# Performance work log

Measured on AMD Instinct MI355X. Metric: run time of the kernel, lower is better.

The kernel has to match this reference:

```python
import jax, jax.numpy as jnp
import numpy as np

EPS = 0.001
WEIGHT = 1.0


def _grid_sample_zeros(x, grid):
    """Bilinear grid_sample, align_corners=True, zeros padding.
    x: [B,C,H,W], grid: [B,H,W,2] in [-1,1] (x then y). Returns [B,C,H,W]."""
    B, C, H, W = x.shape
    gx = (grid[..., 0] + 1.0) * 0.5 * (W - 1)  # [B,H,W] pixel coords
    gy = (grid[..., 1] + 1.0) * 0.5 * (H - 1)
    x0 = jnp.floor(gx)
    y0 = jnp.floor(gy)
    x1 = x0 + 1.0
    y1 = y0 + 1.0
    wx1 = gx - x0
    wx0 = 1.0 - wx1
    wy1 = gy - y0
    wy0 = 1.0 - wy1

    def corner(xi, yi, w):
        valid = ((xi >= 0) & (xi <= W - 1) & (yi >= 0) & (yi <= H - 1)).astype(x.dtype)
        xc = jnp.clip(xi.astype(jnp.int32), 0, W - 1)
        yc = jnp.clip(yi.astype(jnp.int32), 0, H - 1)
        vals = jax.vmap(lambda img, yy, xx: img[:, yy, xx])(x, yc, xc)  # [B,C,H,W]
        return vals * (w * valid)[:, None, :, :]

    return (corner(x0, y0, wx0 * wy0) + corner(x1, y0, wx1 * wy0)
            + corner(x0, y1, wx0 * wy1) + corner(x1, y1, wx1 * wy1))


def _warp(x, flo):
    """Warp x by flow flo (pixel units), with validity mask. x,flo: [B,*,H,W]."""
    B, C, H, W = x.shape
    xx = jnp.arange(W, dtype=x.dtype)[None, :]  # [1,W]
    yy = jnp.arange(H, dtype=x.dtype)[:, None]  # [H,1]
    grid = jnp.stack([jnp.broadcast_to(xx, (H, W)), jnp.broadcast_to(yy, (H, W))], 0)  # [2,H,W]
    vgrid = grid[None] + flo  # [B,2,H,W]
    vx = 2.0 * vgrid[:, 0] / max(W - 1, 1) - 1.0
    vy = 2.0 * vgrid[:, 1] / max(H - 1, 1) - 1.0
    vgrid_n = jnp.stack([vx, vy], -1)  # [B,H,W,2]
    out = _grid_sample_zeros(x, vgrid_n)
    ones = jnp.ones_like(x)
    mask = _grid_sample_zeros(ones, vgrid_n)
    mask = jnp.where(mask < 0.9999, 0.0, 1.0).astype(x.dtype)
    mask = jax.lax.stop_gradient(mask)  # torch writes constants in-place -> no grad
    return out * mask


def setup_inputs() -> dict:
    key = jax.random.key(0)
    k1, k2 = jax.random.split(key)
    N, H, W = 16, 768, 768
    UV_AtoB = jax.random.normal(k1, (N, 2, H, W), dtype=jnp.float32)
    UV_BtoA = jax.random.normal(k2, (N, 2, H, W), dtype=jnp.float32)
    return {"UV_AtoB": UV_AtoB, "UV_BtoA": UV_BtoA}


def reference(UV_AtoB, UV_BtoA):
    N, C, H, W = UV_AtoB.shape
    xx = jnp.broadcast_to(jnp.arange(W, dtype=jnp.float32)[None, :], (H, W))
    yy = jnp.broadcast_to(jnp.arange(H, dtype=jnp.float32)[:, None], (H, W))
    GridXY = jnp.stack([xx / max(W - 1, 1), yy / max(H - 1, 1)], 0)  # [2,H,W]
    GridXY = jnp.broadcast_to(GridXY[None], (N, 2, H, W))

    def cycle_loss(flo1, flo2):
        m = _warp(GridXY, flo1)
        m = _warp(m, flo2)
        diff = jnp.sqrt(jnp.sum((GridXY - m) ** 2, axis=1) + EPS ** 2)  # [N,H,W]
        per = jnp.sum(diff, axis=(1, 2)) / (H * W)
        return jnp.sum(per) / N

    totloss_ABA = cycle_loss(UV_AtoB, UV_BtoA)
    totloss_BAB = cycle_loss(UV_BtoA, UV_AtoB)
    return (totloss_BAB + totloss_ABA) * WEIGHT
```

## Files before the change

### kernel.cpp

```cpp
#include <hip/hip_runtime.h>

constexpr int N = 16, H = 768, W = 768;
constexpr int HW = H * W;
constexpr float EPS2 = 1.0e-6f;
constexpr float INV_W1 = 1.0f / (float)(W - 1);
constexpr float INV_H1 = 1.0f / (float)(H - 1);
constexpr float WM1 = (float)(W - 1);
constexpr float HM1 = (float)(H - 1);
constexpr float WM2 = (float)(W - 2);

constexpr int TILE_COLS = 80;
constexpr int TILE_ROWS = 17;
constexpr int C_HALO = 8;
constexpr int R_HALO = 4;
constexpr int LSTRIDE = TILE_COLS;
constexpr int TILE_FLOATS = TILE_ROWS * LSTRIDE * 2;
constexpr int NBLK_X = W / 64, NBLK_Y = H / 8;
constexpr int NBLOCKS = NBLK_X * NBLK_Y * N;

typedef float float2a __attribute__((ext_vector_type(2), aligned(4)));

struct DirMeta { float gx, gy; int xb, y0, y1; };

__device__ __forceinline__ void dir_meta(float fx, float fy, float xf, float yf, DirMeta& m) {
    m.gx = xf + fx;
    m.gy = yf + fy;
    float x0f = floorf(m.gx);
    float y0f = floorf(m.gy);
    m.xb = (int)fminf(fmaxf(x0f, 0.0f), WM2);
    m.y0 = (int)fminf(fmaxf(y0f, 0.0f), HM1);
    m.y1 = (int)fminf(fmaxf(y0f + 1.0f, 0.0f), HM1);
}

__device__ __forceinline__ bool fast_ok(const DirMeta& m,
                                        float2 u0, float2 v0, float2 u1, float2 v1) {
    float x0f = floorf(m.gx), y0f = floorf(m.gy);
    float a = v0.x + 1.0f, b = v1.x + 1.0f;
    float xmn = fminf(fminf(u0.x, u1.x), fminf(a, b));
    float xmx = fmaxf(fmaxf(u0.x, u1.x), fmaxf(a, b));
    float c = u1.y + 1.0f, d = v1.y + 1.0f;
    float ymn = fminf(fminf(u0.y, v0.y), fminf(c, d));
    float ymx = fmaxf(fmaxf(u0.y, v0.y), fmaxf(c, d));
    return (x0f >= 0.0f) & (x0f <= WM2) & (y0f >= 0.0f) & (y0f <= HM1 - 1.0f)
         & (x0f + xmn >= 0.0f) & (x0f + xmx <= WM1)
         & (y0f + ymn >= 0.0f) & (y0f + ymx <= HM1);
}

__device__ __forceinline__ float fast_eval(const DirMeta& m,
                                           float2 u0, float2 v0, float2 u1, float2 v1,
                                           float fxc, float fyc) {
    float x0f = floorf(m.gx), y0f = floorf(m.gy);
    float wx1 = m.gx - x0f, wy1 = m.gy - y0f;
    float ftx = fmaf(wx1, v0.x - u0.x, u0.x);
    float fty = fmaf(wx1, v0.y - u0.y, u0.y);
    float fbx = fmaf(wx1, v1.x - u1.x, u1.x);
    float fby = fmaf(wx1, v1.y - u1.y, u1.y);
    float fvx = fmaf(wy1, fbx - ftx, ftx);
    float fvy = fmaf(wy1, fby - fty, fty);
    float a = (fxc + fvx) * INV_W1;
    float b = (fyc + fvy) * INV_H1;
    return sqrtf(fmaf(a, a, fmaf(b, b, EPS2)));
}

__device__ __forceinline__ float2 wg(float fx, float fy, float xi, float yi) {
    float gx = xi + fx, gy = yi + fy;
    float x0 = floorf(gx), y0 = floorf(gy);
    float wx1 = gx - x0, wx0 = 1.0f - wx1;
    float wy1 = gy - y0, wy0 = 1.0f - wy1;
    float vx0 = (x0 >= 0.0f  && x0 <= WM1)        ? 1.0f : 0.0f;
    float vx1 = (x0 >= -1.0f && x0 <= WM1 - 1.0f) ? 1.0f : 0.0f;
    float vy0 = (y0 >= 0.0f  && y0 <= HM1)        ? 1.0f : 0.0f;
    float vy1 = (y0 >= -1.0f && y0 <= HM1 - 1.0f) ? 1.0f : 0.0f;
    float ax = wx0 * vx0, bx = wx1 * vx1, sx = ax + bx;
    float ay = wy0 * vy0, by = wy1 * vy1, sy = ay + by;
    float ms = sx * sy;
    float kx = (ms >= 0.9999f) ? INV_W1 : 0.0f;
    float ky = (ms >= 0.9999f) ? INV_H1 : 0.0f;
    float2 r;
    r.x = fmaf(sx, x0, bx) * sy * kx;
    r.y = fmaf(sy, y0, by) * sx * ky;
    return r;
}

__device__ __forceinline__ float dir_eval(const DirMeta& m,
                                          float2 u0, float2 v0, float2 u1, float2 v1,
                                          int x, int y) {
    float x0f = floorf(m.gx), y0f = floorf(m.gy);
    float wx1 = m.gx - x0f, wx0 = 1.0f - wx1;
    float wy1 = m.gy - y0f, wy0 = 1.0f - wy1;
    float x1f = x0f + 1.0f, y1f = y0f + 1.0f;
    float vx0 = (x0f >= 0.0f && x0f <= WM1) ? 1.0f : 0.0f;
    float vx1 = (x1f >= 0.0f && x1f <= WM1) ? 1.0f : 0.0f;
    float vy0 = (y0f >= 0.0f && y0f <= HM1) ? 1.0f : 0.0f;
    float vy1 = (y1f >= 0.0f && y1f <= HM1) ? 1.0f : 0.0f;
    float axw = wx0 * vx0, bxw = wx1 * vx1;
    float ayw = wy0 * vy0, byw = wy1 * vy1;
    float sxw = axw + bxw, syw = ayw + byw;
    float msum = sxw * syw;

    bool selA = (x0f >= WM1);
    bool selB = (x0f >= 0.0f);
    float fx00 = selA ? v0.x : u0.x;
    float fx01 = selB ? v0.x : u0.x;
    float fy00 = selA ? v0.y : u0.y;
    float fy01 = selB ? v0.y : u0.y;
    float fx10 = selA ? v1.x : u1.x;
    float fx11 = selB ? v1.x : u1.x;
    float fy10 = selA ? v1.y : u1.y;
    float fy11 = selB ? v1.y : u1.y;

    float x0c = fminf(fmaxf(x0f, 0.0f), WM1);
    float x1c = fminf(fmaxf(x1f, 0.0f), WM1);
    float y0c = fminf(fmaxf(y0f, 0.0f), HM1);
    float y1c = fminf(fmaxf(y1f, 0.0f), HM1);

    float2 m00 = wg(fx00, fy00, x0c, y0c);
    float2 m01 = wg(fx01, fy01, x1c, y0c);
    float2 m10 = wg(fx10, fy10, x0c, y1c);
    float2 m11 = wg(fx11, fy11, x1c, y1c);

    float w00 = axw * ayw, w10 = bxw * ayw, w01 = axw * byw, w11 = bxw * byw;
    float mx = w00 * m00.x + w10 * m01.x + w01 * m10.x + w11 * m11.x;
    float my = w00 * m00.y + w10 * m01.y + w01 * m10.y + w11 * m11.y;
    float keep = (msum >= 0.9999f) ? 1.0f : 0.0f;
    mx *= keep; my *= keep;

    float dx = (float)x * INV_W1 - mx;
    float dy = (float)y * INV_H1 - my;
    return sqrtf(fmaf(dx, dx, fmaf(dy, dy, EPS2)));
}

__device__ __forceinline__ void ld_quad(const float* t, int pix, float2& u, float2& v) {
    u = *(const float2*)(t + 2 * pix);
    v = *(const float2*)(t + 2 * pix + 2);
}

__global__ __launch_bounds__(256, 7)
void cycle_loss_kernel(const float* __restrict__ A,
                       const float* __restrict__ B,
                       float* __restrict__ ws,
                       float* __restrict__ out,
                       int use_ws) {
    __shared__ float lds[2 * TILE_FLOATS];
    __shared__ float wsum[4];

    int tid  = threadIdx.x;
    int lane = tid & 63;
    int wv   = tid >> 6;
    int bx0 = blockIdx.x * 64;
    int by0 = blockIdx.y * 8;
    int b   = blockIdx.z;
    const float* Ab = A + (size_t)b * 2 * HW;
    const float* Bb = B + (size_t)b * 2 * HW;
    int tc0 = bx0 - C_HALO;
    int tr0 = by0 - R_HALO;

    constexpr int ROW_CHUNKS = TILE_COLS / 4;
    constexpr int TASKS_PER_T = TILE_ROWS * ROW_CHUNKS;
    for (int i = tid; i < 2 * TASKS_PER_T; i += 256) {
        int t   = i / TASKS_PER_T;
        int rem = i - t * TASKS_PER_T;
        int lr  = rem / ROW_CHUNKS;
        int lc4 = rem - lr * ROW_CHUNKS;
        int rg = tr0 + lr;
        int cg = tc0 + lc4 * 4;
        if ((unsigned)rg < (unsigned)H && (unsigned)cg < (unsigned)W) {
            const float* src = (t ? Bb : Ab) + rg * W + cg;
            float4 fx = *(const float4*)(src);
            float4 fy = *(const float4*)(src + HW);
            float* dst = &lds[t * TILE_FLOATS + (lr * LSTRIDE + lc4 * 4) * 2];
            *(float4*)(dst)     = make_float4(fx.x, fy.x, fx.y, fy.y);
            *(float4*)(dst + 4) = make_float4(fx.z, fy.z, fx.w, fy.w);
        }
    }
    __syncthreads();

    const float* ldsA = lds;
    const float* ldsB = lds + TILE_FLOATS;
    int x  = bx0 + lane;
    int yb = by0 + wv * 2;
    int lxc = lane + C_HALO;
    float xf = (float)x;

    float2 aC[2], bC[2];
    #pragma unroll
    for (int p = 0; p < 2; ++p) {
        int co = (wv * 2 + p + R_HALO) * LSTRIDE + lxc;
        aC[p] = *(const float2*)(ldsA + 2 * co);
        bC[p] = *(const float2*)(ldsB + 2 * co);
    }

    float s = 0.0f;
    #pragma unroll
    for (int p = 0; p < 2; ++p) {
        int y = yb + p;
        float yf = (float)y;
        DirMeta m1, m2;
        dir_meta(bC[p].x, bC[p].y, xf, yf, m1);
        dir_meta(aC[p].x, aC[p].y, xf, yf, m2);

        int x1l = m1.xb - tc0, y1l0 = m1.y0 - tr0, y1l1 = m1.y1 - tr0;
        int x2l = m2.xb - tc0, y2l0 = m2.y0 - tr0, y2l1 = m2.y1 - tr0;
        bool e1 = ((unsigned)x1l <= (unsigned)(TILE_COLS - 2))
                & ((unsigned)y1l0 < (unsigned)TILE_ROWS)
                & ((unsigned)y1l1 < (unsigned)TILE_ROWS);
        bool e2 = ((unsigned)x2l <= (unsigned)(TILE_COLS - 2))
                & ((unsigned)y2l0 < (unsigned)TILE_ROWS)
                & ((unsigned)y2l1 < (unsigned)TILE_ROWS);

        float2 u10, v10, u11, v11, u20, v20, u21, v21;
        if (__all(e1 & e2)) {
            ld_quad(ldsA, y1l0 * LSTRIDE + x1l, u10, v10);
            ld_quad(ldsA, y1l1 * LSTRIDE + x1l, u11, v11);
            ld_quad(ldsB, y2l0 * LSTRIDE + x2l, u20, v20);
            ld_quad(ldsB, y2l1 * LSTRIDE + x2l, u21, v21);
        } else {
            if (e1) {
                ld_quad(ldsA, y1l0 * LSTRIDE + x1l, u10, v10);
                ld_quad(ldsA, y1l1 * LSTRIDE + x1l, u11, v11);
            } else {
                int o0 = m1.y0 * W + m1.xb, o1 = m1.y1 * W + m1.xb;
                float2a rx0 = *(const float2a*)(Ab + o0);
                float2a ry0 = *(const float2a*)(Ab + HW + o0);
                float2a rx1 = *(const float2a*)(Ab + o1);
                float2a ry1 = *(const float2a*)(Ab + HW + o1);
                u10 = make_float2(rx0.x, ry0.x); v10 = make_float2(rx0.y, ry0.y);
                u11 = make_float2(rx1.x, ry1.x); v11 = make_float2(rx1.y, ry1.y);
            }
            if (e2) {
                ld_quad(ldsB, y2l0 * LSTRIDE + x2l, u20, v20);
                ld_quad(ldsB, y2l1 * LSTRIDE + x2l, u21, v21);
            } else {
                int o0 = m2.y0 * W + m2.xb, o1 = m2.y1 * W + m2.xb;
                float2a rx0 = *(const float2a*)(Bb + o0);
                float2a ry0 = *(const float2a*)(Bb + HW + o0);
                float2a rx1 = *(const float2a*)(Bb + o1);
                float2a ry1 = *(const float2a*)(Bb + HW + o1);
                u20 = make_float2(rx0.x, ry0.x); v20 = make_float2(rx0.y, ry0.y);
                u21 = make_float2(rx1.x, ry1.x); v21 = make_float2(rx1.y, ry1.y);
            }
        }

        bool ok = fast_ok(m1, u10, v10, u11, v11)
                & fast_ok(m2, u20, v20, u21, v21);
        if (__all(ok)) {
            s += fast_eval(m1, u10, v10, u11, v11, bC[p].x, bC[p].y);
            s += fast_eval(m2, u20, v20, u21, v21, aC[p].x, aC[p].y);
        } else {
            s += dir_eval(m1, u10, v10, u11, v11, x, y);
            s += dir_eval(m2, u20, v20, u21, v21, x, y);
        }
    }

    #pragma unroll
    for (int o = 32; o > 0; o >>= 1) s += __shfl_down(s, o, 64);
    if (lane == 0) wsum[wv] = s;
    __syncthreads();
    if (tid == 0) {
        float tsum = wsum[0] + wsum[1] + wsum[2] + wsum[3];
        if (use_ws) {
            int bid = (blockIdx.z * gridDim.y + blockIdx.y) * gridDim.x + blockIdx.x;
            ws[bid] = tsum;
        } else {
            atomicAdd(out, tsum * (1.0f / ((float)N * (float)H * (float)W)));
        }
    }
}

__global__ __launch_bounds__(256)
void reduce_kernel(const float* __restrict__ ws, float* __restrict__ out) {
    float s = 0.0f;
    for (int i = threadIdx.x; i < NBLOCKS; i += 256) s += ws[i];
    #pragma unroll
    for (int o = 32; o > 0; o >>= 1) s += __shfl_down(s, o, 64);
    __shared__ float wsum[4];
    int lane = threadIdx.x & 63, wv = threadIdx.x >> 6;
    if (lane == 0) wsum[wv] = s;
    __syncthreads();
    if (threadIdx.x == 0) {
        float t = wsum[0] + wsum[1] + wsum[2] + wsum[3];
        out[0] = t * (1.0f / ((float)N * (float)H * (float)W));
    }
}

extern "C" void kernel_launch(void* const* d_in, const int* in_sizes, int n_in,
                              void* d_out, int out_size, void* d_ws, size_t ws_size,
                              hipStream_t stream) {
    const float* A = (const float*)d_in[0];
    const float* B = (const float*)d_in[1];
    float* out = (float*)d_out;
    float* ws  = (float*)d_ws;

    int use_ws = (ws_size >= NBLOCKS * sizeof(float)) ? 1 : 0;
    if (!use_ws) hipMemsetAsync(out, 0, sizeof(float), stream);

    dim3 grid(NBLK_X, NBLK_Y, N);
    cycle_loss_kernel<<<grid, 256, 0, stream>>>(A, B, ws, out, use_ws);
    if (use_ws) reduce_kernel<<<1, 256, 0, stream>>>(ws, out);
}
```

Measured before the change: 224.3 us.

## Process 16 rows per block, vectorize math with float2 types, simplify fast bounds check

Each block now covers 16 rows instead of 8, with each wave handling 4 rows, so the LDS tile grows from 17 to 24 rows and the halo overhead per output pixel shrinks. The fast-path bounds test is rewritten as centered absolute-value comparisons, and the interpolation math uses 2-wide vector types, which may map to packed FP32 instructions. The occupancy hint in launch bounds is dropped and the reduce kernel reads float4. The cost is fewer blocks and more registers per thread, which could lower occupancy and latency hiding.

```diff
diff --git a/kernel.cpp b/kernel.cpp
--- a/kernel.cpp
+++ b/kernel.cpp
@@ -3,63 +3,60 @@
 constexpr int N = 16, H = 768, W = 768;
 constexpr int HW = H * W;
 constexpr float EPS2 = 1.0e-6f;
-constexpr float INV_W1 = 1.0f / (float)(W - 1);
-constexpr float INV_H1 = 1.0f / (float)(H - 1);
-constexpr float WM1 = (float)(W - 1);
-constexpr float HM1 = (float)(H - 1);
-constexpr float WM2 = (float)(W - 2);
+constexpr float INV = 1.0f / 767.0f;
+constexpr float WM1 = 767.0f, WM2 = 766.0f, HM1 = 767.0f;
+constexpr float CHALF  = 383.5f;
+constexpr float CHALFI = 383.0f;
 
 constexpr int TILE_COLS = 80;
-constexpr int TILE_ROWS = 17;
+constexpr int TILE_ROWS = 24;
 constexpr int C_HALO = 8;
 constexpr int R_HALO = 4;
 constexpr int LSTRIDE = TILE_COLS;
 constexpr int TILE_FLOATS = TILE_ROWS * LSTRIDE * 2;
-constexpr int NBLK_X = W / 64, NBLK_Y = H / 8;
+constexpr int NBLK_X = W / 64, NBLK_Y = H / 16;
 constexpr int NBLOCKS = NBLK_X * NBLK_Y * N;
 
+typedef float v2f __attribute__((ext_vector_type(2)));
 typedef float float2a __attribute__((ext_vector_type(2), aligned(4)));
 
-struct DirMeta { float gx, gy; int xb, y0, y1; };
-
-__device__ __forceinline__ void dir_meta(float fx, float fy, float xf, float yf, DirMeta& m) {
-    m.gx = xf + fx;
-    m.gy = yf + fy;
-    float x0f = floorf(m.gx);
-    float y0f = floorf(m.gy);
-    m.xb = (int)fminf(fmaxf(x0f, 0.0f), WM2);
-    m.y0 = (int)fminf(fmaxf(y0f, 0.0f), HM1);
-    m.y1 = (int)fminf(fmaxf(y0f + 1.0f, 0.0f), HM1);
-}
-
-__device__ __forceinline__ bool fast_ok(const DirMeta& m,
-                                        float2 u0, float2 v0, float2 u1, float2 v1) {
-    float x0f = floorf(m.gx), y0f = floorf(m.gy);
-    float a = v0.x + 1.0f, b = v1.x + 1.0f;
-    float xmn = fminf(fminf(u0.x, u1.x), fminf(a, b));
-    float xmx = fmaxf(fmaxf(u0.x, u1.x), fmaxf(a, b));
-    float c = u1.y + 1.0f, d = v1.y + 1.0f;
-    float ymn = fminf(fminf(u0.y, v0.y), fminf(c, d));
-    float ymx = fmaxf(fmaxf(u0.y, v0.y), fmaxf(c, d));
-    return (x0f >= 0.0f) & (x0f <= WM2) & (y0f >= 0.0f) & (y0f <= HM1 - 1.0f)
-         & (x0f + xmn >= 0.0f) & (x0f + xmx <= WM1)
-         & (y0f + ymn >= 0.0f) & (y0f + ymx <= HM1);
+struct DirMeta { v2f g; v2f f0; int xb, y0, y1; };
+
+__device__ __forceinline__ void dir_meta(v2f flow, v2f xy, DirMeta& m) {
+    m.g = xy + flow;
+    m.f0 = (v2f){floorf(m.g.x), floorf(m.g.y)};
+    m.xb = (int)fminf(fmaxf(m.f0.x, 0.0f), WM2);
+    m.y0 = (int)fminf(fmaxf(m.f0.y, 0.0f), HM1);
+    m.y1 = (int)fminf(fmaxf(m.f0.y + 1.0f, 0.0f), HM1);
+}
+
+__device__ __forceinline__ bool fast_ok(v2f f0, v2f u0, v2f v0, v2f u1, v2f v1) {
+    v2f c  = f0 - CHALF;
+    v2f c1 = c + 1.0f;
+    v2f d00 = c  + u0;
+    v2f d11 = c1 + v1;
+    float d01x = c1.x + v0.x, d01y = c.y  + v0.y;
+    float d10x = c.x  + u1.x, d10y = c1.y + u1.y;
+    float xm = fmaxf(fabsf(d00.x), fabsf(d01x));
+    xm = fmaxf(xm, fmaxf(fabsf(d10x), fabsf(d11.x)));
+    float ym = fmaxf(fabsf(d00.y), fabsf(d01y));
+    ym = fmaxf(ym, fmaxf(fabsf(d10y), fabsf(d11.y)));
+    v2f t = c + 0.5f;
+    return (xm <= CHALF) & (ym <= CHALF)
+         & (fabsf(t.x) <= CHALFI) & (fabsf(t.y) <= CHALFI);
 }
 
 __device__ __forceinline__ float fast_eval(const DirMeta& m,
-                                           float2 u0, float2 v0, float2 u1, float2 v1,
-                                           float fxc, float fyc) {
-    float x0f = floorf(m.gx), y0f = floorf(m.gy);
-    float wx1 = m.gx - x0f, wy1 = m.gy - y0f;
-    float ftx = fmaf(wx1, v0.x - u0.x, u0.x);
-    float fty = fmaf(wx1, v0.y - u0.y, u0.y);
-    float fbx = fmaf(wx1, v1.x - u1.x, u1.x);
-    float fby = fmaf(wx1, v1.y - u1.y, u1.y);
-    float fvx = fmaf(wy1, fbx - ftx, ftx);
-    float fvy = fmaf(wy1, fby - fty, fty);
-    float a = (fxc + fvx) * INV_W1;
-    float b = (fyc + fvy) * INV_H1;
-    return sqrtf(fmaf(a, a, fmaf(b, b, EPS2)));
+                                           v2f u0, v2f v0, v2f u1, v2f v1,
+                                           v2f cen) {
+    v2f w = m.g - m.f0;
+    v2f wx = (v2f){w.x, w.x};
+    v2f wy = (v2f){w.y, w.y};
+    v2f ft = u0 + wx * (v0 - u0);
+    v2f fb = u1 + wx * (v1 - u1);
+    v2f fv = ft + wy * (fb - ft);
+    v2f r = (cen + fv) * INV;
+    return sqrtf(fmaf(r.x, r.x, fmaf(r.y, r.y, EPS2)));
 }
 
 __device__ __forceinline__ float2 wg(float fx, float fy, float xi, float yi) {
@@ -74,8 +71,8 @@
     float ax = wx0 * vx0, bx = wx1 * vx1, sx = ax + bx;
     float ay = wy0 * vy0, by = wy1 * vy1, sy = ay + by;
     float ms = sx * sy;
-    float kx = (ms >= 0.9999f) ? INV_W1 : 0.0f;
-    float ky = (ms >= 0.9999f) ? INV_H1 : 0.0f;
+    float kx = (ms >= 0.9999f) ? INV : 0.0f;
+    float ky = (ms >= 0.9999f) ? INV : 0.0f;
     float2 r;
     r.x = fmaf(sx, x0, bx) * sy * kx;
     r.y = fmaf(sy, y0, by) * sx * ky;
@@ -83,11 +80,11 @@
 }
 
 __device__ __forceinline__ float dir_eval(const DirMeta& m,
-                                          float2 u0, float2 v0, float2 u1, float2 v1,
-                                          int x, int y) {
-    float x0f = floorf(m.gx), y0f = floorf(m.gy);
-    float wx1 = m.gx - x0f, wx0 = 1.0f - wx1;
-    float wy1 = m.gy - y0f, wy0 = 1.0f - wy1;
+                                          v2f u0, v2f v0, v2f u1, v2f v1,
+                                          float xf, float yf) {
+    float x0f = m.f0.x, y0f = m.f0.y;
+    float wx1 = m.g.x - x0f, wx0 = 1.0f - wx1;
+    float wy1 = m.g.y - y0f, wy0 = 1.0f - wy1;
     float x1f = x0f + 1.0f, y1f = y0f + 1.0f;
     float vx0 = (x0f >= 0.0f && x0f <= WM1) ? 1.0f : 0.0f;
     float vx1 = (x1f >= 0.0f && x1f <= WM1) ? 1.0f : 0.0f;
@@ -125,17 +122,17 @@
     float keep = (msum >= 0.9999f) ? 1.0f : 0.0f;
     mx *= keep; my *= keep;
 
-    float dx = (float)x * INV_W1 - mx;
-    float dy = (float)y * INV_H1 - my;
+    float dx = xf * INV - mx;
+    float dy = yf * INV - my;
     return sqrtf(fmaf(dx, dx, fmaf(dy, dy, EPS2)));
 }
 
-__device__ __forceinline__ void ld_quad(const float* t, int pix, float2& u, float2& v) {
-    u = *(const float2*)(t + 2 * pix);
-    v = *(const float2*)(t + 2 * pix + 2);
-}
-
-__global__ __launch_bounds__(256, 7)
+__device__ __forceinline__ void ld_quad(const float* t, int pix, v2f& u, v2f& v) {
+    u = *(const v2f*)(t + 2 * pix);
+    v = *(const v2f*)(t + 2 * pix + 2);
+}
+
+__global__ __launch_bounds__(256)
 void cycle_loss_kernel(const float* __restrict__ A,
                        const float* __restrict__ B,
                        float* __restrict__ ws,
@@ -148,7 +145,7 @@
     int lane = tid & 63;
     int wv   = tid >> 6;
     int bx0 = blockIdx.x * 64;
-    int by0 = blockIdx.y * 8;
+    int by0 = blockIdx.y * 16;
     int b   = blockIdx.z;
     const float* Ab = A + (size_t)b * 2 * HW;
     const float* Bb = B + (size_t)b * 2 * HW;
@@ -178,26 +175,26 @@
     const float* ldsA = lds;
     const float* ldsB = lds + TILE_FLOATS;
     int x  = bx0 + lane;
-    int yb = by0 + wv * 2;
+    int yb = by0 + wv * 4;
     int lxc = lane + C_HALO;
     float xf = (float)x;
 
-    float2 aC[2], bC[2];
+    v2f aC[4], bC[4];
     #pragma unroll
-    for (int p = 0; p < 2; ++p) {
-        int co = (wv * 2 + p + R_HALO) * LSTRIDE + lxc;
-        aC[p] = *(const float2*)(ldsA + 2 * co);
-        bC[p] = *(const float2*)(ldsB + 2 * co);
+    for (int p = 0; p < 4; ++p) {
+        int co = (wv * 4 + p + R_HALO) * LSTRIDE + lxc;
+        aC[p] = *(const v2f*)(ldsA + 2 * co);
+        bC[p] = *(const v2f*)(ldsB + 2 * co);
     }
 
     float s = 0.0f;
     #pragma unroll
-    for (int p = 0; p < 2; ++p) {
-        int y = yb + p;
-        float yf = (float)y;
+    for (int p = 0; p < 4; ++p) {
+        float yf = (float)(yb + p);
+        v2f xy = (v2f){xf, yf};
         DirMeta m1, m2;
-        dir_meta(bC[p].x, bC[p].y, xf, yf, m1);
-        dir_meta(aC[p].x, aC[p].y, xf, yf, m2);
+        dir_meta(bC[p], xy, m1);
+        dir_meta(aC[p], xy, m2);
 
         int x1l = m1.xb - tc0, y1l0 = m1.y0 - tr0, y1l1 = m1.y1 - tr0;
         int x2l = m2.xb - tc0, y2l0 = m2.y0 - tr0, y2l1 = m2.y1 - tr0;
@@ -208,7 +205,7 @@
                 & ((unsigned)y2l0 < (unsigned)TILE_ROWS)
                 & ((unsigned)y2l1 < (unsigned)TILE_ROWS);
 
-        float2 u10, v10, u11, v11, u20, v20, u21, v21;
+        v2f u10, v10, u11, v11, u20, v20, u21, v21;
         if (__all(e1 & e2)) {
             ld_quad(ldsA, y1l0 * LSTRIDE + x1l, u10, v10);
             ld_quad(ldsA, y1l1 * LSTRIDE + x1l, u11, v11);
@@ -224,8 +221,8 @@
                 float2a ry0 = *(const float2a*)(Ab + HW + o0);
                 float2a rx1 = *(const float2a*)(Ab + o1);
                 float2a ry1 = *(const float2a*)(Ab + HW + o1);
-                u10 = make_float2(rx0.x, ry0.x); v10 = make_float2(rx0.y, ry0.y);
-                u11 = make_float2(rx1.x, ry1.x); v11 = make_float2(rx1.y, ry1.y);
+                u10 = (v2f){rx0.x, ry0.x}; v10 = (v2f){rx0.y, ry0.y};
+                u11 = (v2f){rx1.x, ry1.x}; v11 = (v2f){rx1.y, ry1.y};
             }
             if (e2) {
                 ld_quad(ldsB, y2l0 * LSTRIDE + x2l, u20, v20);
@@ -236,19 +233,19 @@
                 float2a ry0 = *(const float2a*)(Bb + HW + o0);
                 float2a rx1 = *(const float2a*)(Bb + o1);
                 float2a ry1 = *(const float2a*)(Bb + HW + o1);
-                u20 = make_float2(rx0.x, ry0.x); v20 = make_float2(rx0.y, ry0.y);
-                u21 = make_float2(rx1.x, ry1.x); v21 = make_float2(rx1.y, ry1.y);
+                u20 = (v2f){rx0.x, ry0.x}; v20 = (v2f){rx0.y, ry0.y};
+                u21 = (v2f){rx1.x, ry1.x}; v21 = (v2f){rx1.y, ry1.y};
             }
         }
 
-        bool ok = fast_ok(m1, u10, v10, u11, v11)
-                & fast_ok(m2, u20, v20, u21, v21);
+        bool ok = fast_ok(m1.f0, u10, v10, u11, v11)
+                & fast_ok(m2.f0, u20, v20, u21, v21);
         if (__all(ok)) {
-            s += fast_eval(m1, u10, v10, u11, v11, bC[p].x, bC[p].y);
-            s += fast_eval(m2, u20, v20, u21, v21, aC[p].x, aC[p].y);
+            s += fast_eval(m1, u10, v10, u11, v11, bC[p]);
+            s += fast_eval(m2, u20, v20, u21, v21, aC[p]);
         } else {
-            s += dir_eval(m1, u10, v10, u11, v11, x, y);
-            s += dir_eval(m2, u20, v20, u21, v21, x, y);
+            s += dir_eval(m1, u10, v10, u11, v11, xf, yf);
+            s += dir_eval(m2, u20, v20, u21, v21, xf, yf);
         }
     }
 
@@ -270,7 +267,10 @@
 __global__ __launch_bounds__(256)
 void reduce_kernel(const float* __restrict__ ws, float* __restrict__ out) {
     float s = 0.0f;
-    for (int i = threadIdx.x; i < NBLOCKS; i += 256) s += ws[i];
+    for (int i = threadIdx.x; i < NBLOCKS / 4; i += 256) {
+        float4 v = *(const float4*)(ws + 4 * i);
+        s += (v.x + v.y) + (v.z + v.w);
+    }
     #pragma unroll
     for (int o = 32; o > 0; o >>= 1) s += __shfl_down(s, o, 64);
     __shared__ float wsum[4];
```

Measured after the change: 202.1 us. 1.11x faster.
